# Kernel optimization log

Hardware: AMD Instinct MI355X
Metric: run time of the kernel (lower is better)

The kernel has to match this reference:

```python
import jax, jax.numpy as jnp
import numpy as np
from jax import lax

B, N, C = 256, 256, 192
HEADS = 6
HD = C // HEADS
WIN = 16
AGENT = 49
POOL = 7            # int(agent_num ** 0.5)
SCALE = HD ** -0.5


def _pool_matrix(inn, out):
    # PyTorch AdaptiveAvgPool2d bin edges: start=floor(i*inn/out), end=ceil((i+1)*inn/out)
    P = np.zeros((out, inn), np.float32)
    for i in range(out):
        s = (i * inn) // out
        e = -(((-(i + 1)) * inn) // out)
        P[i, s:e] = 1.0 / (e - s)
    return jnp.asarray(P)

_P = _pool_matrix(WIN, POOL)  # (7, 16) adaptive-avg-pool operator


def _resize_bilinear(x, out_h, out_w):
    # matches F.interpolate(mode='bilinear', align_corners=False)
    H, W = x.shape[-2], x.shape[-1]
    def idx(out, inn):
        s = (jnp.arange(out, dtype=jnp.float32) + 0.5) * (inn / out) - 0.5
        s = jnp.maximum(s, 0.0)
        i0 = jnp.minimum(jnp.floor(s).astype(jnp.int32), inn - 1)
        i1 = jnp.minimum(i0 + 1, inn - 1)
        return i0, i1, s - i0.astype(jnp.float32)
    h0, h1, th = idx(out_h, H)
    w0, w1, tw = idx(out_w, W)
    xh = x[..., h0, :] * (1.0 - th)[:, None] + x[..., h1, :] * th[:, None]
    return xh[..., :, w0] * (1.0 - tw) + xh[..., :, w1] * tw


def setup_inputs() -> dict:
    key = jax.random.key(0)
    ks = jax.random.split(key, 18)
    lin = lambda k: jax.random.normal(k, (C, C), jnp.float32) * 0.02
    zc = jnp.zeros((C,), jnp.float32)
    tn = lambda k, shp: jax.random.normal(k, shp, jnp.float32) * 0.02
    return {
        "x_F1": jax.random.normal(ks[0], (B, N, C), jnp.float32),
        "x_C2": jax.random.normal(ks[1], (B, N, C), jnp.float32),
        "x_C1": jax.random.normal(ks[2], (B, N, C), jnp.float32),
        "Wq": lin(ks[3]), "bq": zc,
        "Wk": lin(ks[4]), "bk": zc,
        "Wv": lin(ks[5]), "bv": zc,
        "Wa1": lin(ks[6]), "ba1": zc,
        "Wa2": lin(ks[7]), "ba2": zc,
        "an_bias": tn(ks[8], (HEADS, AGENT, 7, 7)),
        "na_bias": tn(ks[9], (HEADS, AGENT, 7, 7)),
        "ah_bias": tn(ks[10], (1, HEADS, AGENT, WIN, 1)),
        "aw_bias": tn(ks[11], (1, HEADS, AGENT, 1, WIN)),
        "ha_bias": tn(ks[12], (1, HEADS, WIN, 1, AGENT)),
        "wa_bias": tn(ks[13], (1, HEADS, 1, WIN, AGENT)),
        "dwc_w": tn(ks[14], (C, 1, 3, 3)),
        "dwc_b": zc,
        "Wp": lin(ks[15]), "bp": zc,
    }


def reference(x_F1, x_C2, x_C1, Wq, bq, Wk, bk, Wv, bv, Wa1, ba1, Wa2, ba2,
              an_bias, na_bias, ah_bias, aw_bias, ha_bias, wa_bias,
              dwc_w, dwc_b, Wp, bp):
    b, n, c = x_F1.shape
    h = w = WIN
    q = x_F1 @ Wq.T + bq
    k = (x_F1 + x_C2 - x_C1) @ Wk.T + bk
    v = (x_C2 - x_C1) @ Wv.T + bv
    # agent tokens: linear -> adaptive avg pool 16x16 -> 7x7 -> (b, 49, c)
    a1 = (x_C1 @ Wa1.T + ba1).reshape(b, h, w, c)
    a1 = jnp.einsum('ph,bhwc,qw->bpqc', _P, a1, _P).reshape(b, AGENT, c)
    a2 = (x_C2 @ Wa2.T + ba2).reshape(b, h, w, c)
    a2 = jnp.einsum('ph,bhwc,qw->bpqc', _P, a2, _P).reshape(b, AGENT, c)
    qh = q.reshape(b, n, HEADS, HD).transpose(0, 2, 1, 3)
    kh = k.reshape(b, n, HEADS, HD).transpose(0, 2, 1, 3)
    vh = v.reshape(b, n, HEADS, HD).transpose(0, 2, 1, 3)
    a1h = a1.reshape(b, AGENT, HEADS, HD).transpose(0, 2, 1, 3)
    a2h = a2.reshape(b, AGENT, HEADS, HD).transpose(0, 2, 1, 3)
    # stage 1: agent <- k/v attention, bias = interp(an_bias) + (ah+aw)
    pb = (_resize_bilinear(an_bias, h, w).reshape(1, HEADS, AGENT, n)
          + (ah_bias + aw_bias).reshape(1, HEADS, AGENT, n))
    attn2 = jax.nn.softmax(SCALE * jnp.einsum('bhad,bhnd->bhan', a2h, kh) + pb, axis=-1)
    agent_v = jnp.einsum('bhan,bhnd->bhad', attn2, vh)
    # stage 2: query <- agent attention, bias = interp(na_bias)^T + (ha+wa)
    ab = (jnp.swapaxes(_resize_bilinear(na_bias, h, w).reshape(HEADS, AGENT, n), -1, -2)[None]
          + (ha_bias + wa_bias).reshape(1, HEADS, n, AGENT))
    q_attn = jax.nn.softmax(SCALE * jnp.einsum('bhnd,bhad->bhna', qh, a1h) + ab, axis=-1)
    x = jnp.einsum('bhna,bhad->bhnd', q_attn, agent_v).transpose(0, 2, 1, 3).reshape(b, n, c)
    # depthwise 3x3 conv on q as spatial map
    q_img = q.reshape(b, h, w, c).transpose(0, 3, 1, 2)
    dw = lax.conv_general_dilated(q_img, dwc_w, (1, 1), ((1, 1), (1, 1)),
                                  feature_group_count=c,
                                  dimension_numbers=('NCHW', 'OIHW', 'NCHW'))
    dw = dw + dwc_b.reshape(1, c, 1, 1)
    x = x + dw.transpose(0, 2, 3, 1).reshape(b, n, c)
    return x @ Wp.T + bp
```

## Files before the change

### kernel.cpp

```cpp
#include <hip/hip_runtime.h>

typedef __bf16 bf16;
typedef __bf16 bf16x4 __attribute__((ext_vector_type(4)));
typedef __bf16 bf16x8 __attribute__((ext_vector_type(8)));
typedef float  f32x4  __attribute__((ext_vector_type(4)));

#define DEVI __device__ __forceinline__

static constexpr int   BATCH = 256;
static constexpr int   SEQ   = 256;
static constexpr int   CH    = 192;
static constexpr int   NH    = 6;
static constexpr int   AG    = 49;
static constexpr float QK_SCALE = 0.17677669529663687f;

__device__ constexpr int   PPN[16]  = {1,1,2,1,2,1,2,1,1,2,1,2,1,2,1,1};
__device__ constexpr int   PPB0[16] = {0,0,0,1,1,2,2,3,3,3,4,4,5,5,6,6};
__device__ constexpr int   PPB1[16] = {0,0,1,0,2,0,3,0,0,4,0,5,0,6,0,0};
__device__ constexpr float PPW0[16] = {1.f/3.f,1.f/3.f,1.f/3.f,1.f/3.f,1.f/3.f,1.f/3.f,1.f/3.f,0.25f,0.25f,0.25f,
                                       1.f/3.f,1.f/3.f,1.f/3.f,1.f/3.f,1.f/3.f,1.f/3.f};
__device__ constexpr float PPW1[16] = {0.f,0.f,1.f/3.f,0.f,1.f/3.f,0.f,0.25f,0.f,0.f,1.f/3.f,
                                       0.f,1.f/3.f,0.f,1.f/3.f,0.f,0.f};

#if defined(__has_builtin)
#if __has_builtin(__builtin_amdgcn_global_load_lds)
#define HAVE_GLL 1
#endif
#endif

DEVI void gll16(const void* g, void* l, int lane) {
#ifdef HAVE_GLL
  (void)lane;
  __builtin_amdgcn_global_load_lds(
      (const __attribute__((address_space(1))) void*)g,
      (__attribute__((address_space(3))) void*)l, 16, 0, 0);
#else
  *(uint4*)((char*)l + lane * 16) = *(const uint4*)((const char*)g);
#endif
}

DEVI float bilin7(const float* m, int i, int j) {
  float sh = (i + 0.5f) * 0.4375f - 0.5f; sh = sh < 0.f ? 0.f : sh;
  float sw = (j + 0.5f) * 0.4375f - 0.5f; sw = sw < 0.f ? 0.f : sw;
  int i0 = (int)sh; if (i0 > 6) i0 = 6;
  int j0 = (int)sw; if (j0 > 6) j0 = 6;
  int i1 = i0 + 1;  if (i1 > 6) i1 = 6;
  int j1 = j0 + 1;  if (j1 > 6) j1 = 6;
  float th = sh - (float)i0, tw = sw - (float)j0;
  float v00 = m[i0*7 + j0], v01 = m[i0*7 + j1];
  float v10 = m[i1*7 + j0], v11 = m[i1*7 + j1];
  return (v00*(1.f-tw) + v01*tw)*(1.f-th) + (v10*(1.f-tw) + v11*tw)*th;
}

__global__ void k_prep(const float* Wq, const float* Wk, const float* Wv,
                       const float* Wa1, const float* Wa2, const float* Wp,
                       const float* an_bias, const float* na_bias,
                       const float* ah_bias, const float* aw_bias,
                       const float* ha_bias, const float* wa_bias,
                       bf16* wsW, float* pb, float* ab, bf16* a1, bf16* a2) {
  int gid = blockIdx.x * 256 + threadIdx.x;
  if (gid < 221184) {
    int mi = gid / 36864, r = gid - mi * 36864;
    const float* W = (mi == 0 ? Wq : mi == 1 ? Wk : mi == 2 ? Wv :
                      mi == 3 ? Wa1 : mi == 4 ? Wa2 : Wp);
    wsW[gid] = (bf16)W[r];
  } else if (gid < 296448) {
    int r = gid - 221184;
    int n = r & 255, ha = r >> 8;
    int i = n >> 4, j = n & 15;
    float val = bilin7(an_bias + (size_t)ha * 49, i, j)
              + ah_bias[ha * 16 + i] + aw_bias[ha * 16 + j];
    pb[r] = val;
  } else if (gid < 371712) {
    int r = gid - 296448;
    int a = r % 49, hn = r / 49;
    int n = hn & 255, hh = hn >> 8;
    int i = n >> 4, j = n & 15;
    float val = bilin7(na_bias + (size_t)(hh * 49 + a) * 49, i, j)
              + ha_bias[(hh * 16 + i) * 49 + a] + wa_bias[(hh * 16 + j) * 49 + a];
    ab[r] = val;
  } else if (gid < 396288) {
    int r = gid - 371712;
    if (r < 12288) a1[(size_t)12544 * CH + r] = (bf16)0.f;
    else           a2[(size_t)12544 * CH + (r - 12288)] = (bf16)0.f;
  }
}

__global__ __launch_bounds__(256, 2) void k_qkv(
    const float* xF1, const float* xC2, const float* xC1,
    const bf16* wsW, const float* bq, const float* bk, const float* bv,
    bf16* qO, bf16* kO, bf16* vO) {
  __shared__ char L[73728] __attribute__((aligned(16)));
  const int tid = threadIdx.x, lane = tid & 63, wid = tid >> 6;
  const int l15 = lane & 15, lg = lane >> 4;
  const int m0 = blockIdx.x * 32;

  {
    const char* s0 = (const char*)(xF1 + (size_t)m0 * CH);
    const char* s1 = (const char*)(xC2 + (size_t)m0 * CH);
    const char* s2 = (const char*)(xC1 + (size_t)m0 * CH);
    #pragma unroll
    for (int i = 0; i < 6; ++i) {
      const int off = (wid * 6 + i) * 1024;
      gll16(s0 + off + lane * 16, L + off, lane);
    }
    #pragma unroll
    for (int i = 0; i < 6; ++i) {
      const int off = (wid * 6 + i) * 1024;
      gll16(s1 + off + lane * 16, L + 24576 + off, lane);
    }
    #pragma unroll
    for (int i = 0; i < 6; ++i) {
      const int off = (wid * 6 + i) * 1024;
      gll16(s2 + off + lane * 16, L + 49152 + off, lane);
    }
  }
  __syncthreads();

  {
    float vF[24], v2[24], v1[24];
    #pragma unroll
    for (int g = 0; g < 6; ++g) {
      const int byt = (tid + 256 * g) * 16;
      *(float4*)&vF[4 * g] = *(const float4*)(L + byt);
      *(float4*)&v2[4 * g] = *(const float4*)(L + 24576 + byt);
      *(float4*)&v1[4 * g] = *(const float4*)(L + 49152 + byt);
    }
    __syncthreads();
    #pragma unroll
    for (int g = 0; g < 6; ++g) {
      bf16x4 tq, tk, tv;
      #pragma unroll
      for (int e = 0; e < 4; ++e) {
        const float f = vF[4 * g + e];
        const float d = v2[4 * g + e] - v1[4 * g + e];
        tq[e] = (bf16)f;
        tk[e] = (bf16)(f + d);
        tv[e] = (bf16)d;
      }
      const int f0  = (tid + 256 * g) * 4;
      const int row = f0 / 192, col = f0 - row * 192;
      const int cb2 = col * 2;
      const int byt = row * 384 + ((cb2 & ~15) ^ ((row & 7) << 4)) + (cb2 & 15);
      *(bf16x4*)(L + byt)         = tq;
      *(bf16x4*)(L + 12288 + byt) = tk;
      *(bf16x4*)(L + 24576 + byt) = tv;
    }
  }
  __syncthreads();

  #pragma unroll 1
  for (int job = 0; job < 3; ++job) {
    const bf16*  Wj   = wsW + job * 36864;
    const float* bias = (job == 0 ? bq : job == 1 ? bk : bv);
    bf16*        outp = (job == 0 ? qO : job == 1 ? kO : vO);
    const char*  T    = L + job * 12288;

    f32x4 acc[2][3];
    #pragma unroll
    for (int rt = 0; rt < 2; ++rt)
      #pragma unroll
      for (int ct = 0; ct < 3; ++ct) acc[rt][ct] = f32x4{0.f, 0.f, 0.f, 0.f};

    #pragma unroll
    for (int kk = 0; kk < 6; ++kk) {
      bf16x8 af[2];
      #pragma unroll
      for (int rt = 0; rt < 2; ++rt) {
        const int row = 16 * rt + l15;
        af[rt] = *(const bf16x8*)(T + row * 384 + ((kk * 64 + lg * 16) ^ ((row & 7) << 4)));
      }
      #pragma unroll
      for (int ct = 0; ct < 3; ++ct) {
        const int ncol = 48 * wid + 16 * ct + l15;
        bf16x8 bfr = *(const bf16x8*)&Wj[(size_t)ncol * CH + kk * 32 + 8 * lg];
        acc[0][ct] = __builtin_amdgcn_mfma_f32_16x16x32_bf16(af[0], bfr, acc[0][ct], 0, 0, 0);
        acc[1][ct] = __builtin_amdgcn_mfma_f32_16x16x32_bf16(af[1], bfr, acc[1][ct], 0, 0, 0);
      }
    }
    __syncthreads();
    #pragma unroll
    for (int ct = 0; ct < 3; ++ct) {
      const int col = 48 * wid + 16 * ct + l15;
      const float bb = bias[col];
      #pragma unroll
      for (int rt = 0; rt < 2; ++rt)
        #pragma unroll
        for (int r = 0; r < 4; ++r) {
          const int row = 16 * rt + 4 * lg + r;
          *(bf16*)(L + 36864 + row * 400 + col * 2) = (bf16)(acc[rt][ct][r] + bb);
        }
    }
    __syncthreads();
    #pragma unroll
    for (int v = 0; v < 3; ++v) {
      const int c   = tid + 256 * v;
      const int row = c / 24;
      const int y   = (c - row * 24) * 16;
      bf16x8 vv = *(const bf16x8*)(L + 36864 + row * 400 + y);
      *(bf16x8*)((char*)outp + (size_t)(m0 + row) * 384 + y) = vv;
    }
  }
}

__global__ __launch_bounds__(192) void k_pool(
    const float* xC1, const float* xC2, bf16* pooled1, bf16* pooled2) {
  const int b = blockIdx.x, which = blockIdx.y, c = threadIdx.x;
  const float* src = (which ? xC2 : xC1) + (size_t)b * SEQ * CH + c;
  bf16* dst = (which ? pooled2 : pooled1) + (size_t)b * AG * CH + c;
  float acc[49];
  #pragma unroll
  for (int a = 0; a < 49; ++a) acc[a] = 0.f;
  #pragma unroll
  for (int i = 0; i < 16; ++i) {
    float jq[7] = {0.f, 0.f, 0.f, 0.f, 0.f, 0.f, 0.f};
    #pragma unroll
    for (int j = 0; j < 16; ++j) {
      const float x = src[(i * 16 + j) * CH];
      jq[PPB0[j]] += PPW0[j] * x;
      if (PPN[j] == 2) jq[PPB1[j]] += PPW1[j] * x;
    }
    {
      const int p0 = PPB0[i]; const float w0 = PPW0[i];
      #pragma unroll
      for (int qq = 0; qq < 7; ++qq) acc[p0 * 7 + qq] += w0 * jq[qq];
    }
    if (PPN[i] == 2) {
      const int p1 = PPB1[i]; const float w1 = PPW1[i];
      #pragma unroll
      for (int qq = 0; qq < 7; ++qq) acc[p1 * 7 + qq] += w1 * jq[qq];
    }
  }
  #pragma unroll
  for (int a = 0; a < 49; ++a) dst[(size_t)a * CH + c] = (bf16)acc[a];
}

DEVI void gemm_body(const bf16* Asrc, const bf16* W, const float* bias,
                    bf16* outp, int m0, bf16 (*sA)[72]) {
  const int tid = threadIdx.x, lane = tid & 63, wid = tid >> 6;
  const int l15 = lane & 15, lg = lane >> 4;
  const int wr = wid >> 1, wc = wid & 1;
  const int srow = tid >> 1, shalf = tid & 1;

  f32x4 acc[4][6];
  #pragma unroll
  for (int a = 0; a < 4; ++a)
    #pragma unroll
    for (int b2 = 0; b2 < 6; ++b2) acc[a][b2] = f32x4{0.f, 0.f, 0.f, 0.f};

  for (int ks = 0; ks < 3; ++ks) {
    const int k0 = ks * 64;
    const uint4* src = (const uint4*)(Asrc + (size_t)(m0 + srow) * CH + k0 + shalf * 32);
    #pragma unroll
    for (int i2 = 0; i2 < 4; ++i2)
      *(uint4*)&sA[srow][shalf * 32 + 8 * i2] = src[i2];
    __syncthreads();
    #pragma unroll
    for (int kk = 0; kk < 64; kk += 32) {
      bf16x8 af[4];
      #pragma unroll
      for (int rt = 0; rt < 4; ++rt)
        af[rt] = *(const bf16x8*)&sA[64 * wr + 16 * rt + l15][kk + 8 * lg];
      #pragma unroll
      for (int ct = 0; ct < 6; ++ct) {
        const int ncol = 96 * wc + 16 * ct + l15;
        bf16x8 bfr = *(const bf16x8*)&W[(size_t)ncol * CH + k0 + kk + 8 * lg];
        #pragma unroll
        for (int rt = 0; rt < 4; ++rt)
          acc[rt][ct] = __builtin_amdgcn_mfma_f32_16x16x32_bf16(af[rt], bfr, acc[rt][ct], 0, 0, 0);
      }
    }
    __syncthreads();
  }
  #pragma unroll
  for (int ct = 0; ct < 6; ++ct) {
    const int col = 96 * wc + 16 * ct + l15;
    const float bb = bias[col];
    #pragma unroll
    for (int rt = 0; rt < 4; ++rt) {
      const size_t rbase = (size_t)(m0 + 64 * wr + 16 * rt + 4 * lg);
      #pragma unroll
      for (int r = 0; r < 4; ++r)
        outp[(rbase + r) * CH + col] = (bf16)(acc[rt][ct][r] + bb);
    }
  }
}

__global__ __launch_bounds__(256, 2) void k_gemm2(
    const bf16* pooled1, const bf16* pooled2, const bf16* wsW,
    const float* ba1, const float* ba2, bf16* a1, bf16* a2) {
  __shared__ bf16 sA[128][72] __attribute__((aligned(16)));
  const int m0 = blockIdx.x * 128;
  if (blockIdx.y == 0) gemm_body(pooled1, wsW + 3 * 36864, ba1, a1, m0, sA);
  else                 gemm_body(pooled2, wsW + 4 * 36864, ba2, a2, m0, sA);
}

__global__ __launch_bounds__(256, 3) void k_gemm_out(
    const bf16* xsum, const bf16* Wp, const float* bp, float* out) {
  __shared__ char sA[49152] __attribute__((aligned(16)));
  const int tid = threadIdx.x, lane = tid & 63, wid = tid >> 6;
  const int l15 = lane & 15, lg = lane >> 4;
  const int wr = wid >> 1, wc = wid & 1;
  const int m0 = blockIdx.x * 128;

  {
    const char* gsrc = (const char*)xsum + (size_t)m0 * 384;
    #pragma unroll
    for (int i = 0; i < 12; ++i) {
      const int off = (wid * 12 + i) * 1024;
      gll16(gsrc + off + lane * 16, sA + off, lane);
    }
  }
  __syncthreads();

  f32x4 acc[4][6];
  #pragma unroll
  for (int a = 0; a < 4; ++a)
    #pragma unroll
    for (int b2 = 0; b2 < 6; ++b2) acc[a][b2] = f32x4{0.f, 0.f, 0.f, 0.f};

  #pragma unroll
  for (int kk = 0; kk < 6; ++kk) {
    bf16x8 af[4];
    #pragma unroll
    for (int rt = 0; rt < 4; ++rt) {
      const int row = 64 * wr + 16 * rt + l15;
      af[rt] = *(const bf16x8*)(sA + row * 384 + ((kk * 64 + lg * 16) ^ ((row & 7) << 4)));
    }
    #pragma unroll
    for (int ct = 0; ct < 6; ++ct) {
      const int ncol = 96 * wc + 16 * ct + l15;
      bf16x8 bfr = *(const bf16x8*)&Wp[(size_t)ncol * CH + kk * 32 + 8 * lg];
      #pragma unroll
      for (int rt = 0; rt < 4; ++rt)
        acc[rt][ct] = __builtin_amdgcn_mfma_f32_16x16x32_bf16(af[rt], bfr, acc[rt][ct], 0, 0, 0);
    }
  }
  #pragma unroll
  for (int ct = 0; ct < 6; ++ct) {
    const int col = 96 * wc + 16 * ct + l15;
    const float bb = bp[col];
    #pragma unroll
    for (int rt = 0; rt < 4; ++rt)
      #pragma unroll
      for (int r = 0; r < 4; ++r)
        out[(size_t)(m0 + 64 * wr + 16 * rt + 4 * lg + r) * CH + col] = acc[rt][ct][r] + bb;
  }
}

__global__ __launch_bounds__(256, 2) void k_attn(
    const bf16* q, const bf16* k, const bf16* v,
    const bf16* a1, const bf16* a2, const float* pb, const float* ab,
    const float* dwc_w, const float* dwc_b, bf16* xsum) {
  const int h = blockIdx.x, b = blockIdx.y;
  __shared__ char uSmem[36864] __attribute__((aligned(16)));
  bf16 (*log1)[264] = reinterpret_cast<bf16 (*)[264]>(uSmem);
  bf16 (*log2)[72]  = reinterpret_cast<bf16 (*)[72]>(uSmem);
  __shared__ bf16 sVT[32][264] __attribute__((aligned(16)));
  __shared__ bf16 sAVT[32][72] __attribute__((aligned(16)));
  __shared__ float srow1[64];
  __shared__ float srow2[256];
  __shared__ bf16 xat[256][36] __attribute__((aligned(16)));
  __shared__ float sW[9][32];
  __shared__ float dwb[32];

  const int tid = threadIdx.x, lane = tid & 63, wv = tid >> 6;
  const int l15 = lane & 15, lg = lane >> 4;

  const bf16* qb  = q  + (size_t)b * SEQ * CH + h * 32;
  const bf16* kb  = k  + (size_t)b * SEQ * CH + h * 32;
  const bf16* vb  = v  + (size_t)b * SEQ * CH + h * 32;
  const bf16* a1b = a1 + (size_t)b * AG  * CH + h * 32;
  const bf16* a2b = a2 + (size_t)b * AG  * CH + h * 32;

  for (int idx = tid; idx < 288; idx += 256) {
    const int cl = idx / 9, tap = idx - cl * 9;
    sW[tap][cl] = dwc_w[(32 * h + cl) * 9 + tap];
  }
  if (tid < 32) dwb[tid] = dwc_b[32 * h + tid];

  {
    const int p = tid & 127, dg = tid >> 7;
    const bf16* s0 = vb + (size_t)(2 * p) * CH + dg * 16;
    bf16x8 r0a = ((const bf16x8*)s0)[0];
    bf16x8 r0b = ((const bf16x8*)s0)[1];
    bf16x8 r1a = ((const bf16x8*)(s0 + CH))[0];
    bf16x8 r1b = ((const bf16x8*)(s0 + CH))[1];
    #pragma unroll
    for (int j = 0; j < 8; ++j) {
      union { bf16 e[2]; unsigned u; } u0, u1;
      u0.e[0] = r0a[j]; u0.e[1] = r1a[j];
      u1.e[0] = r0b[j]; u1.e[1] = r1b[j];
      *(unsigned*)&sVT[dg * 16 + j][2 * p]     = u0.u;
      *(unsigned*)&sVT[dg * 16 + 8 + j][2 * p] = u1.u;
    }
  }

  {
    bf16x8 afr[4];
    #pragma unroll
    for (int rt = 0; rt < 4; ++rt)
      afr[rt] = *(const bf16x8*)(a2b + (size_t)(16 * rt + l15) * CH + 8 * lg);
    #pragma unroll
    for (int ct = 0; ct < 4; ++ct) {
      const int n = 64 * wv + 16 * ct + l15;
      bf16x8 bfr = *(const bf16x8*)(kb + (size_t)n * CH + 8 * lg);
      #pragma unroll
      for (int rt = 0; rt < 4; ++rt) {
        f32x4 acc = {0.f, 0.f, 0.f, 0.f};
        acc = __builtin_amdgcn_mfma_f32_16x16x32_bf16(afr[rt], bfr, acc, 0, 0, 0);
        #pragma unroll
        for (int r = 0; r < 4; ++r)
          log1[16 * rt + 4 * lg + r][n] = (bf16)acc[r];
      }
    }
  }
  __syncthreads();

  if (tid < 196) {
    const int a = tid >> 2, qu = tid & 3;
    const float* pbrow = pb + ((size_t)h * AG + a) * SEQ + qu * 64;
    float vbuf[64];
    float m = -1e30f;
    #pragma unroll
    for (int i2 = 0; i2 < 8; ++i2) {
      bf16x8 raw = *(const bf16x8*)&log1[a][qu * 64 + 8 * i2];
      #pragma unroll
      for (int j = 0; j < 8; ++j) {
        float x = QK_SCALE * (float)raw[j] + pbrow[8 * i2 + j];
        vbuf[8 * i2 + j] = x;
        m = fmaxf(m, x);
      }
    }
    m = fmaxf(m, __shfl_xor(m, 1));
    m = fmaxf(m, __shfl_xor(m, 2));
    float s = 0.f;
    #pragma unroll
    for (int i2 = 0; i2 < 8; ++i2) {
      bf16x8 eb;
      #pragma unroll
      for (int j = 0; j < 8; ++j) {
        float e = __expf(vbuf[8 * i2 + j] - m);
        s += e;
        eb[j] = (bf16)e;
      }
      *(bf16x8*)&log1[a][qu * 64 + 8 * i2] = eb;
    }
    s += __shfl_xor(s, 1);
    s += __shfl_xor(s, 2);
    if (qu == 0) srow1[a] = 1.f / s;
  }
  __syncthreads();

  {
    f32x4 acc0 = {0.f, 0.f, 0.f, 0.f}, acc1 = {0.f, 0.f, 0.f, 0.f};
    #pragma unroll
    for (int ksn = 0; ksn < 8; ++ksn) {
      bf16x8 af = *(const bf16x8*)&log1[16 * wv + l15][32 * ksn + 8 * lg];
      bf16x8 b0 = *(const bf16x8*)&sVT[l15][32 * ksn + 8 * lg];
      bf16x8 b1 = *(const bf16x8*)&sVT[16 + l15][32 * ksn + 8 * lg];
      acc0 = __builtin_amdgcn_mfma_f32_16x16x32_bf16(af, b0, acc0, 0, 0, 0);
      acc1 = __builtin_amdgcn_mfma_f32_16x16x32_bf16(af, b1, acc1, 0, 0, 0);
    }
    #pragma unroll
    for (int r = 0; r < 4; ++r) {
      const int a = 16 * wv + 4 * lg + r;
      const float inv = (a < AG) ? srow1[a] : 0.f;
      sAVT[l15][a]      = (bf16)(acc0[r] * inv);
      sAVT[16 + l15][a] = (bf16)(acc1[r] * inv);
    }
  }
  __syncthreads();

  {
    bf16x8 bfr[4];
    #pragma unroll
    for (int ct = 0; ct < 4; ++ct)
      bfr[ct] = *(const bf16x8*)(a1b + (size_t)(16 * ct + l15) * CH + 8 * lg);
    #pragma unroll
    for (int rt = 0; rt < 4; ++rt) {
      bf16x8 af = *(const bf16x8*)(qb + (size_t)(64 * wv + 16 * rt + l15) * CH + 8 * lg);
      #pragma unroll
      for (int ct = 0; ct < 4; ++ct) {
        f32x4 acc = {0.f, 0.f, 0.f, 0.f};
        acc = __builtin_amdgcn_mfma_f32_16x16x32_bf16(af, bfr[ct], acc, 0, 0, 0);
        #pragma unroll
        for (int r = 0; r < 4; ++r)
          log2[64 * wv + 16 * rt + 4 * lg + r][16 * ct + l15] = (bf16)acc[r];
      }
    }
  }
  __syncthreads();

  {
    const float* abrow = ab + ((size_t)h * SEQ + tid) * AG;
    float vb2[49];
    float m = -1e30f;
    #pragma unroll
    for (int i2 = 0; i2 < 6; ++i2) {
      bf16x8 raw = *(const bf16x8*)&log2[tid][8 * i2];
      #pragma unroll
      for (int j = 0; j < 8; ++j) {
        float x = QK_SCALE * (float)raw[j] + abrow[8 * i2 + j];
        vb2[8 * i2 + j] = x;
        m = fmaxf(m, x);
      }
    }
    {
      float x = QK_SCALE * (float)log2[tid][48] + abrow[48];
      vb2[48] = x;
      m = fmaxf(m, x);
    }
    float s = 0.f;
    #pragma unroll
    for (int i2 = 0; i2 < 8; ++i2) {
      bf16x8 eb;
      #pragma unroll
      for (int j = 0; j < 8; ++j) {
        const int idx = 8 * i2 + j;
        float e = 0.f;
        if (idx < AG) { e = __expf(vb2[idx] - m); }
        s += e;
        eb[j] = (bf16)e;
      }
      *(bf16x8*)&log2[tid][8 * i2] = eb;
    }
    srow2[tid] = 1.f / s;
  }
  __syncthreads();

  {
    bf16x8 bfr[2][2];
    #pragma unroll
    for (int ksn = 0; ksn < 2; ++ksn) {
      bfr[ksn][0] = *(const bf16x8*)&sAVT[l15][32 * ksn + 8 * lg];
      bfr[ksn][1] = *(const bf16x8*)&sAVT[16 + l15][32 * ksn + 8 * lg];
    }
    #pragma unroll
    for (int rt = 0; rt < 4; ++rt) {
      f32x4 acc0 = {0.f, 0.f, 0.f, 0.f}, acc1 = {0.f, 0.f, 0.f, 0.f};
      #pragma unroll
      for (int ksn = 0; ksn < 2; ++ksn) {
        bf16x8 af = *(const bf16x8*)&log2[64 * wv + 16 * rt + l15][32 * ksn + 8 * lg];
        acc0 = __builtin_amdgcn_mfma_f32_16x16x32_bf16(af, bfr[ksn][0], acc0, 0, 0, 0);
        acc1 = __builtin_amdgcn_mfma_f32_16x16x32_bf16(af, bfr[ksn][1], acc1, 0, 0, 0);
      }
      #pragma unroll
      for (int r = 0; r < 4; ++r) {
        const int nq = 64 * wv + 16 * rt + 4 * lg + r;
        const float inv = srow2[nq];
        xat[nq][l15]      = (bf16)(acc0[r] * inv);
        xat[nq][16 + l15] = (bf16)(acc1[r] * inv);
      }
    }
  }
  __syncthreads();

  {
    const int n = tid, ii = n >> 4, jj = n & 15;
    float acc[32];
    #pragma unroll
    for (int u = 0; u < 4; ++u) {
      bf16x4 xa0 = *(const bf16x4*)&xat[n][8 * u];
      bf16x4 xa1 = *(const bf16x4*)&xat[n][8 * u + 4];
      #pragma unroll
      for (int e = 0; e < 4; ++e) {
        acc[8 * u + e]     = dwb[8 * u + e]     + (float)xa0[e];
        acc[8 * u + 4 + e] = dwb[8 * u + 4 + e] + (float)xa1[e];
      }
    }
    #pragma unroll
    for (int di = 0; di < 3; ++di) {
      const int i2 = ii + di - 1;
      if ((unsigned)i2 >= 16u) continue;
      #pragma unroll
      for (int dj = 0; dj < 3; ++dj) {
        const int j2 = jj + dj - 1;
        if ((unsigned)j2 >= 16u) continue;
        const int tap = di * 3 + dj;
        const bf16* qr = q + ((size_t)b * SEQ + i2 * 16 + j2) * CH + h * 32;
        #pragma unroll
        for (int u = 0; u < 4; ++u) {
          bf16x8 qv = *(const bf16x8*)(qr + 8 * u);
          const float4* wv4 = (const float4*)&sW[tap][8 * u];
          float4 wa = wv4[0], wb2 = wv4[1];
          acc[8*u+0] += (float)qv[0] * wa.x;  acc[8*u+1] += (float)qv[1] * wa.y;
          acc[8*u+2] += (float)qv[2] * wa.z;  acc[8*u+3] += (float)qv[3] * wa.w;
          acc[8*u+4] += (float)qv[4] * wb2.x; acc[8*u+5] += (float)qv[5] * wb2.y;
          acc[8*u+6] += (float)qv[6] * wb2.z; acc[8*u+7] += (float)qv[7] * wb2.w;
        }
      }
    }
    char* xo = (char*)xsum + (size_t)(b * SEQ + n) * 384;
    const int sw = (n & 7) << 4;
    #pragma unroll
    for (int u = 0; u < 4; ++u) {
      bf16x8 ob;
      #pragma unroll
      for (int e = 0; e < 8; ++e) ob[e] = (bf16)acc[8 * u + e];
      *(bf16x8*)(xo + ((64 * h + 16 * u) ^ sw)) = ob;
    }
  }
}

extern "C" void kernel_launch(void* const* d_in, const int* in_sizes, int n_in,
                              void* d_out, int out_size, void* d_ws, size_t ws_size,
                              hipStream_t stream) {
  (void)in_sizes; (void)n_in; (void)out_size; (void)ws_size;
  const float* xF1 = (const float*)d_in[0];
  const float* xC2 = (const float*)d_in[1];
  const float* xC1 = (const float*)d_in[2];
  const float* Wq  = (const float*)d_in[3];
  const float* bq  = (const float*)d_in[4];
  const float* Wk  = (const float*)d_in[5];
  const float* bk  = (const float*)d_in[6];
  const float* Wv  = (const float*)d_in[7];
  const float* bv  = (const float*)d_in[8];
  const float* Wa1 = (const float*)d_in[9];
  const float* ba1 = (const float*)d_in[10];
  const float* Wa2 = (const float*)d_in[11];
  const float* ba2 = (const float*)d_in[12];
  const float* an_bias = (const float*)d_in[13];
  const float* na_bias = (const float*)d_in[14];
  const float* ah_bias = (const float*)d_in[15];
  const float* aw_bias = (const float*)d_in[16];
  const float* ha_bias = (const float*)d_in[17];
  const float* wa_bias = (const float*)d_in[18];
  const float* dwc_w = (const float*)d_in[19];
  const float* dwc_b = (const float*)d_in[20];
  const float* Wp  = (const float*)d_in[21];
  const float* bp  = (const float*)d_in[22];

  char* ws = (char*)d_ws;
  size_t off = 0;
  auto nxt = [&](size_t bytes) -> char* {
    char* p = ws + off;
    off = (off + bytes + 255) & ~(size_t)255;
    return p;
  };
  const size_t XSZ = (size_t)BATCH * SEQ * CH;
  const size_t ASZ = ((size_t)BATCH * AG + 64) * CH;

  bf16*  wsW     = (bf16*)nxt(6 * 36864 * sizeof(bf16));
  float* pb      = (float*)nxt(6 * 49 * 256 * sizeof(float));
  float* ab      = (float*)nxt(6 * 256 * 49 * sizeof(float));
  bf16*  pooled1 = (bf16*)nxt(ASZ * sizeof(bf16));
  bf16*  pooled2 = (bf16*)nxt(ASZ * sizeof(bf16));
  bf16*  qB      = (bf16*)nxt(XSZ * sizeof(bf16));
  bf16*  kB      = (bf16*)nxt(XSZ * sizeof(bf16));
  bf16*  vB      = (bf16*)nxt(XSZ * sizeof(bf16));
  bf16*  a1B     = (bf16*)nxt(ASZ * sizeof(bf16));
  bf16*  a2B     = (bf16*)nxt(ASZ * sizeof(bf16));
  bf16*  xsum    = (bf16*)nxt(XSZ * sizeof(bf16));

  k_prep<<<1548, 256, 0, stream>>>(Wq, Wk, Wv, Wa1, Wa2, Wp,
                                   an_bias, na_bias, ah_bias, aw_bias,
                                   ha_bias, wa_bias, wsW, pb, ab, a1B, a2B);
  k_qkv<<<2048, 256, 0, stream>>>(xF1, xC2, xC1, wsW, bq, bk, bv, qB, kB, vB);
  k_pool<<<dim3(BATCH, 2), 192, 0, stream>>>(xC1, xC2, pooled1, pooled2);
  k_gemm2<<<dim3(98, 2), 256, 0, stream>>>(pooled1, pooled2, wsW, ba1, ba2, a1B, a2B);
  k_attn<<<dim3(NH, BATCH), 256, 0, stream>>>(qB, kB, vB, a1B, a2B, pb, ab,
                                              dwc_w, dwc_b, xsum);
  k_gemm_out<<<512, 256, 0, stream>>>(xsum, wsW + 5 * 36864, bp, (float*)d_out);
}
```

Baseline: 219.3 us.

## Split QKV projection per job, restructure pooling, store attention biases as bf16

The fused QKV kernel, which staged all three inputs in 72KB of LDS, becomes a per-job projection kernel launched on a 3-deep grid. Each block reads fp32 inputs directly into MFMA fragments and uses a small LDS buffer, which allows higher occupancy. The cost is reading xF1/xC2/xC1 multiple times across jobs. The pooling kernel now processes channel pairs and splits rows across two thread halves, combining them through LDS. The precomputed attention bias tables are stored as bf16 (ab padded to 56) to halve their traffic and allow vector loads, at some precision cost.

```diff
diff --git a/kernel.cpp b/kernel.cpp
--- a/kernel.cpp
+++ b/kernel.cpp
@@ -57,7 +57,7 @@
                        const float* an_bias, const float* na_bias,
                        const float* ah_bias, const float* aw_bias,
                        const float* ha_bias, const float* wa_bias,
-                       bf16* wsW, float* pb, float* ab, bf16* a1, bf16* a2) {
+                       bf16* wsW, bf16* pb, bf16* ab, bf16* a1, bf16* a2) {
   int gid = blockIdx.x * 256 + threadIdx.x;
   if (gid < 221184) {
     int mi = gid / 36864, r = gid - mi * 36864;
@@ -70,169 +70,175 @@
     int i = n >> 4, j = n & 15;
     float val = bilin7(an_bias + (size_t)ha * 49, i, j)
               + ah_bias[ha * 16 + i] + aw_bias[ha * 16 + j];
-    pb[r] = val;
-  } else if (gid < 371712) {
+    pb[r] = (bf16)val;
+  } else if (gid < 382464) {
     int r = gid - 296448;
-    int a = r % 49, hn = r / 49;
+    int a = r % 56, hn = r / 56;
     int n = hn & 255, hh = hn >> 8;
     int i = n >> 4, j = n & 15;
-    float val = bilin7(na_bias + (size_t)(hh * 49 + a) * 49, i, j)
-              + ha_bias[(hh * 16 + i) * 49 + a] + wa_bias[(hh * 16 + j) * 49 + a];
-    ab[r] = val;
-  } else if (gid < 396288) {
-    int r = gid - 371712;
+    float val = 0.f;
+    if (a < AG)
+      val = bilin7(na_bias + (size_t)(hh * 49 + a) * 49, i, j)
+          + ha_bias[(hh * 16 + i) * 49 + a] + wa_bias[(hh * 16 + j) * 49 + a];
+    ab[r] = (bf16)val;
+  } else if (gid < 407040) {
+    int r = gid - 382464;
     if (r < 12288) a1[(size_t)12544 * CH + r] = (bf16)0.f;
     else           a2[(size_t)12544 * CH + (r - 12288)] = (bf16)0.f;
   }
 }
 
-__global__ __launch_bounds__(256, 2) void k_qkv(
+__global__ __launch_bounds__(256, 4) void k_proj(
     const float* xF1, const float* xC2, const float* xC1,
     const bf16* wsW, const float* bq, const float* bk, const float* bv,
     bf16* qO, bf16* kO, bf16* vO) {
-  __shared__ char L[73728] __attribute__((aligned(16)));
+  __shared__ char L[12800] __attribute__((aligned(16)));
   const int tid = threadIdx.x, lane = tid & 63, wid = tid >> 6;
   const int l15 = lane & 15, lg = lane >> 4;
+  const int rh = wid >> 1, chf = wid & 1;
+  const int job = blockIdx.y;
   const int m0 = blockIdx.x * 32;
 
-  {
-    const char* s0 = (const char*)(xF1 + (size_t)m0 * CH);
-    const char* s1 = (const char*)(xC2 + (size_t)m0 * CH);
-    const char* s2 = (const char*)(xC1 + (size_t)m0 * CH);
-    #pragma unroll
-    for (int i = 0; i < 6; ++i) {
-      const int off = (wid * 6 + i) * 1024;
-      gll16(s0 + off + lane * 16, L + off, lane);
-    }
-    #pragma unroll
-    for (int i = 0; i < 6; ++i) {
-      const int off = (wid * 6 + i) * 1024;
-      gll16(s1 + off + lane * 16, L + 24576 + off, lane);
-    }
-    #pragma unroll
-    for (int i = 0; i < 6; ++i) {
-      const int off = (wid * 6 + i) * 1024;
-      gll16(s2 + off + lane * 16, L + 49152 + off, lane);
-    }
-  }
-  __syncthreads();
-
-  {
-    float vF[24], v2[24], v1[24];
-    #pragma unroll
-    for (int g = 0; g < 6; ++g) {
-      const int byt = (tid + 256 * g) * 16;
-      *(float4*)&vF[4 * g] = *(const float4*)(L + byt);
-      *(float4*)&v2[4 * g] = *(const float4*)(L + 24576 + byt);
-      *(float4*)&v1[4 * g] = *(const float4*)(L + 49152 + byt);
-    }
-    __syncthreads();
-    #pragma unroll
-    for (int g = 0; g < 6; ++g) {
-      bf16x4 tq, tk, tv;
-      #pragma unroll
-      for (int e = 0; e < 4; ++e) {
-        const float f = vF[4 * g + e];
-        const float d = v2[4 * g + e] - v1[4 * g + e];
-        tq[e] = (bf16)f;
-        tk[e] = (bf16)(f + d);
-        tv[e] = (bf16)d;
-      }
-      const int f0  = (tid + 256 * g) * 4;
-      const int row = f0 / 192, col = f0 - row * 192;
-      const int cb2 = col * 2;
-      const int byt = row * 384 + ((cb2 & ~15) ^ ((row & 7) << 4)) + (cb2 & 15);
-      *(bf16x4*)(L + byt)         = tq;
-      *(bf16x4*)(L + 12288 + byt) = tk;
-      *(bf16x4*)(L + 24576 + byt) = tv;
-    }
-  }
-  __syncthreads();
-
-  #pragma unroll 1
-  for (int job = 0; job < 3; ++job) {
-    const bf16*  Wj   = wsW + job * 36864;
-    const float* bias = (job == 0 ? bq : job == 1 ? bk : bv);
-    bf16*        outp = (job == 0 ? qO : job == 1 ? kO : vO);
-    const char*  T    = L + job * 12288;
-
-    f32x4 acc[2][3];
-    #pragma unroll
-    for (int rt = 0; rt < 2; ++rt)
-      #pragma unroll
-      for (int ct = 0; ct < 3; ++ct) acc[rt][ct] = f32x4{0.f, 0.f, 0.f, 0.f};
-
-    #pragma unroll
-    for (int kk = 0; kk < 6; ++kk) {
-      bf16x8 af[2];
-      #pragma unroll
-      for (int rt = 0; rt < 2; ++rt) {
-        const int row = 16 * rt + l15;
-        af[rt] = *(const bf16x8*)(T + row * 384 + ((kk * 64 + lg * 16) ^ ((row & 7) << 4)));
-      }
-      #pragma unroll
-      for (int ct = 0; ct < 3; ++ct) {
-        const int ncol = 48 * wid + 16 * ct + l15;
-        bf16x8 bfr = *(const bf16x8*)&Wj[(size_t)ncol * CH + kk * 32 + 8 * lg];
-        acc[0][ct] = __builtin_amdgcn_mfma_f32_16x16x32_bf16(af[0], bfr, acc[0][ct], 0, 0, 0);
-        acc[1][ct] = __builtin_amdgcn_mfma_f32_16x16x32_bf16(af[1], bfr, acc[1][ct], 0, 0, 0);
-      }
-    }
-    __syncthreads();
-    #pragma unroll
-    for (int ct = 0; ct < 3; ++ct) {
-      const int col = 48 * wid + 16 * ct + l15;
-      const float bb = bias[col];
-      #pragma unroll
-      for (int rt = 0; rt < 2; ++rt)
-        #pragma unroll
-        for (int r = 0; r < 4; ++r) {
-          const int row = 16 * rt + 4 * lg + r;
-          *(bf16*)(L + 36864 + row * 400 + col * 2) = (bf16)(acc[rt][ct][r] + bb);
-        }
-    }
-    __syncthreads();
-    #pragma unroll
-    for (int v = 0; v < 3; ++v) {
-      const int c   = tid + 256 * v;
-      const int row = c / 24;
-      const int y   = (c - row * 24) * 16;
-      bf16x8 vv = *(const bf16x8*)(L + 36864 + row * 400 + y);
-      *(bf16x8*)((char*)outp + (size_t)(m0 + row) * 384 + y) = vv;
-    }
-  }
-}
+  const bf16*  Wj   = wsW + job * 36864;
+  const float* bias = (job == 0 ? bq : job == 1 ? bk : bv);
+  bf16*        outp = (job == 0 ? qO : job == 1 ? kO : vO);
+
+  const size_t arow = (size_t)(m0 + 16 * rh + l15) * CH + 8 * lg;
+
+  f32x4 acc[6];
+  #pragma unroll
+  for (int ct = 0; ct < 6; ++ct) acc[ct] = f32x4{0.f, 0.f, 0.f, 0.f};
+
+  #pragma unroll
+  for (int kk = 0; kk < 6; ++kk) {
+    bf16x8 af;
+    if (job == 0) {
+      float f[8];
+      *(float4*)&f[0] = *(const float4*)(xF1 + arow + kk * 32);
+      *(float4*)&f[4] = *(const float4*)(xF1 + arow + kk * 32 + 4);
+      #pragma unroll
+      for (int e = 0; e < 8; ++e) af[e] = (bf16)f[e];
+    } else if (job == 1) {
+      float f[8], c2[8], c1[8];
+      *(float4*)&f[0]  = *(const float4*)(xF1 + arow + kk * 32);
+      *(float4*)&f[4]  = *(const float4*)(xF1 + arow + kk * 32 + 4);
+      *(float4*)&c2[0] = *(const float4*)(xC2 + arow + kk * 32);
+      *(float4*)&c2[4] = *(const float4*)(xC2 + arow + kk * 32 + 4);
+      *(float4*)&c1[0] = *(const float4*)(xC1 + arow + kk * 32);
+      *(float4*)&c1[4] = *(const float4*)(xC1 + arow + kk * 32 + 4);
+      #pragma unroll
+      for (int e = 0; e < 8; ++e) af[e] = (bf16)(f[e] + c2[e] - c1[e]);
+    } else {
+      float c2[8], c1[8];
+      *(float4*)&c2[0] = *(const float4*)(xC2 + arow + kk * 32);
+      *(float4*)&c2[4] = *(const float4*)(xC2 + arow + kk * 32 + 4);
+      *(float4*)&c1[0] = *(const float4*)(xC1 + arow + kk * 32);
+      *(float4*)&c1[4] = *(const float4*)(xC1 + arow + kk * 32 + 4);
+      #pragma unroll
+      for (int e = 0; e < 8; ++e) af[e] = (bf16)(c2[e] - c1[e]);
+    }
+    #pragma unroll
+    for (int ct = 0; ct < 6; ++ct) {
+      const int ncol = 96 * chf + 16 * ct + l15;
+      bf16x8 bfr = *(const bf16x8*)&Wj[(size_t)ncol * CH + kk * 32 + 8 * lg];
+      acc[ct] = __builtin_amdgcn_mfma_f32_16x16x32_bf16(af, bfr, acc[ct], 0, 0, 0);
+    }
+  }
+
+  #pragma unroll
+  for (int ct = 0; ct < 6; ++ct) {
+    const int col = 96 * chf + 16 * ct + l15;
+    const float bb = bias[col];
+    #pragma unroll
+    for (int r = 0; r < 4; ++r)
+      *(bf16*)(L + (16 * rh + 4 * lg + r) * 400 + col * 2) = (bf16)(acc[ct][r] + bb);
+  }
+  __syncthreads();
+  #pragma unroll
+  for (int v = 0; v < 3; ++v) {
+    const int c   = tid + 256 * v;
+    const int row = c / 24;
+    const int y   = (c - row * 24) * 16;
+    *(bf16x8*)((char*)outp + (size_t)(m0 + row) * 384 + y) =
+        *(const bf16x8*)(L + row * 400 + y);
+  }
+}
+
+#define POOLROW(I, P0, W0, P1, W1) do {                                        \
+    float jqx[7] = {0,0,0,0,0,0,0}, jqy[7] = {0,0,0,0,0,0,0};                  \
+    _Pragma("unroll")                                                          \
+    for (int j = 0; j < 16; ++j) {                                             \
+      float2 x = *(const float2*)(src + (size_t)((I) * 16 + j) * CH);          \
+      jqx[PPB0[j]] += PPW0[j] * x.x;  jqy[PPB0[j]] += PPW0[j] * x.y;           \
+      if (PPN[j] == 2) { jqx[PPB1[j]] += PPW1[j] * x.x;                        \
+                         jqy[PPB1[j]] += PPW1[j] * x.y; }                      \
+    }                                                                          \
+    _Pragma("unroll")                                                          \
+    for (int q = 0; q < 7; ++q) { ax[P0][q] += (W0) * jqx[q];                  \
+                                  ay[P0][q] += (W0) * jqy[q]; }                \
+    if ((P1) >= 0) {                                                           \
+      _Pragma("unroll")                                                        \
+      for (int q = 0; q < 7; ++q) { ax[(P1) & 3][q] += (W1) * jqx[q];          \
+                                    ay[(P1) & 3][q] += (W1) * jqy[q]; }        \
+    }                                                                          \
+  } while (0)
 
 __global__ __launch_bounds__(192) void k_pool(
     const float* xC1, const float* xC2, bf16* pooled1, bf16* pooled2) {
-  const int b = blockIdx.x, which = blockIdx.y, c = threadIdx.x;
-  const float* src = (which ? xC2 : xC1) + (size_t)b * SEQ * CH + c;
-  bf16* dst = (which ? pooled2 : pooled1) + (size_t)b * AG * CH + c;
-  float acc[49];
-  #pragma unroll
-  for (int a = 0; a < 49; ++a) acc[a] = 0.f;
-  #pragma unroll
-  for (int i = 0; i < 16; ++i) {
-    float jq[7] = {0.f, 0.f, 0.f, 0.f, 0.f, 0.f, 0.f};
-    #pragma unroll
-    for (int j = 0; j < 16; ++j) {
-      const float x = src[(i * 16 + j) * CH];
-      jq[PPB0[j]] += PPW0[j] * x;
-      if (PPN[j] == 2) jq[PPB1[j]] += PPW1[j] * x;
-    }
-    {
-      const int p0 = PPB0[i]; const float w0 = PPW0[i];
-      #pragma unroll
-      for (int qq = 0; qq < 7; ++qq) acc[p0 * 7 + qq] += w0 * jq[qq];
-    }
-    if (PPN[i] == 2) {
-      const int p1 = PPB1[i]; const float w1 = PPW1[i];
-      #pragma unroll
-      for (int qq = 0; qq < 7; ++qq) acc[p1 * 7 + qq] += w1 * jq[qq];
-    }
-  }
-  #pragma unroll
-  for (int a = 0; a < 49; ++a) dst[(size_t)a * CH + c] = (bf16)acc[a];
+  __shared__ float lred[7][192];
+  const int b = blockIdx.x, which = blockIdx.y, t = threadIdx.x;
+  const int cp = t % 96, ih = t / 96;
+  const float* src = (which ? xC2 : xC1) + (size_t)b * SEQ * CH + 2 * cp;
+  bf16* dst = (which ? pooled2 : pooled1) + (size_t)b * AG * CH + 2 * cp;
+
+  float ax[4][7], ay[4][7];
+  #pragma unroll
+  for (int p = 0; p < 4; ++p)
+    #pragma unroll
+    for (int q = 0; q < 7; ++q) { ax[p][q] = 0.f; ay[p][q] = 0.f; }
+
+  const float TH = 1.f / 3.f, QU = 0.25f;
+  if (ih == 0) {
+    POOLROW(0, 0, TH, -1, 0.f);  POOLROW(1, 0, TH, -1, 0.f);
+    POOLROW(2, 0, TH,  1, TH);   POOLROW(3, 1, TH, -1, 0.f);
+    POOLROW(4, 1, TH,  2, TH);   POOLROW(5, 2, TH, -1, 0.f);
+    POOLROW(6, 2, TH,  3, QU);   POOLROW(7, 3, QU, -1, 0.f);
+  } else {
+    POOLROW(8,  0, QU, -1, 0.f); POOLROW(9,  0, QU,  1, TH);
+    POOLROW(10, 1, TH, -1, 0.f); POOLROW(11, 1, TH,  2, TH);
+    POOLROW(12, 2, TH, -1, 0.f); POOLROW(13, 2, TH,  3, TH);
+    POOLROW(14, 3, TH, -1, 0.f); POOLROW(15, 3, TH, -1, 0.f);
+  }
+  if (ih == 1) {
+    #pragma unroll
+    for (int q = 0; q < 7; ++q) {
+      lred[q][2 * cp] = ax[0][q]; lred[q][2 * cp + 1] = ay[0][q];
+    }
+  }
+  __syncthreads();
+  if (ih == 0) {
+    #pragma unroll
+    for (int q = 0; q < 7; ++q) {
+      ax[3][q] += lred[q][2 * cp]; ay[3][q] += lred[q][2 * cp + 1];
+    }
+    #pragma unroll
+    for (int p = 0; p < 4; ++p)
+      #pragma unroll
+      for (int q = 0; q < 7; ++q) {
+        union { bf16 e[2]; unsigned u; } u;
+        u.e[0] = (bf16)ax[p][q]; u.e[1] = (bf16)ay[p][q];
+        *(unsigned*)&dst[(size_t)(p * 7 + q) * CH] = u.u;
+      }
+  } else {
+    #pragma unroll
+    for (int lp = 1; lp < 4; ++lp)
+      #pragma unroll
+      for (int q = 0; q < 7; ++q) {
+        union { bf16 e[2]; unsigned u; } u;
+        u.e[0] = (bf16)ax[lp][q]; u.e[1] = (bf16)ay[lp][q];
+        *(unsigned*)&dst[(size_t)((3 + lp) * 7 + q) * CH] = u.u;
+      }
+  }
 }
 
 DEVI void gemm_body(const bf16* Asrc, const bf16* W, const float* bias,
@@ -350,7 +356,7 @@
 
 __global__ __launch_bounds__(256, 2) void k_attn(
     const bf16* q, const bf16* k, const bf16* v,
-    const bf16* a1, const bf16* a2, const float* pb, const float* ab,
+    const bf16* a1, const bf16* a2, const bf16* pb, const bf16* ab,
     const float* dwc_w, const float* dwc_b, bf16* xsum) {
   const int h = blockIdx.x, b = blockIdx.y;
   __shared__ char uSmem[36864] __attribute__((aligned(16)));
@@ -419,15 +425,16 @@
 
   if (tid < 196) {
     const int a = tid >> 2, qu = tid & 3;
-    const float* pbrow = pb + ((size_t)h * AG + a) * SEQ + qu * 64;
+    const bf16* pbrow = pb + ((size_t)h * AG + a) * SEQ + qu * 64;
     float vbuf[64];
     float m = -1e30f;
     #pragma unroll
     for (int i2 = 0; i2 < 8; ++i2) {
       bf16x8 raw = *(const bf16x8*)&log1[a][qu * 64 + 8 * i2];
+      bf16x8 pbb = *(const bf16x8*)&pbrow[8 * i2];
       #pragma unroll
       for (int j = 0; j < 8; ++j) {
-        float x = QK_SCALE * (float)raw[j] + pbrow[8 * i2 + j];
+        float x = QK_SCALE * (float)raw[j] + (float)pbb[j];
         vbuf[8 * i2 + j] = x;
         m = fmaxf(m, x);
       }
@@ -493,21 +500,22 @@
   __syncthreads();
 
   {
-    const float* abrow = ab + ((size_t)h * SEQ + tid) * AG;
+    const bf16* abrow = ab + ((size_t)h * SEQ + tid) * 56;
     float vb2[49];
     float m = -1e30f;
     #pragma unroll
     for (int i2 = 0; i2 < 6; ++i2) {
       bf16x8 raw = *(const bf16x8*)&log2[tid][8 * i2];
+      bf16x8 abb = *(const bf16x8*)&abrow[8 * i2];
       #pragma unroll
       for (int j = 0; j < 8; ++j) {
-        float x = QK_SCALE * (float)raw[j] + abrow[8 * i2 + j];
+        float x = QK_SCALE * (float)raw[j] + (float)abb[j];
         vb2[8 * i2 + j] = x;
         m = fmaxf(m, x);
       }
     }
     {
-      float x = QK_SCALE * (float)log2[tid][48] + abrow[48];
+      float x = QK_SCALE * (float)log2[tid][48] + (float)abrow[48];
       vb2[48] = x;
       m = fmaxf(m, x);
     }
@@ -642,8 +650,8 @@
   const size_t ASZ = ((size_t)BATCH * AG + 64) * CH;
 
   bf16*  wsW     = (bf16*)nxt(6 * 36864 * sizeof(bf16));
-  float* pb      = (float*)nxt(6 * 49 * 256 * sizeof(float));
-  float* ab      = (float*)nxt(6 * 256 * 49 * sizeof(float));
+  bf16*  pb      = (bf16*)nxt(6 * 49 * 256 * sizeof(bf16));
+  bf16*  ab      = (bf16*)nxt(6 * 256 * 56 * sizeof(bf16));
   bf16*  pooled1 = (bf16*)nxt(ASZ * sizeof(bf16));
   bf16*  pooled2 = (bf16*)nxt(ASZ * sizeof(bf16));
   bf16*  qB      = (bf16*)nxt(XSZ * sizeof(bf16));
@@ -653,10 +661,11 @@
   bf16*  a2B     = (bf16*)nxt(ASZ * sizeof(bf16));
   bf16*  xsum    = (bf16*)nxt(XSZ * sizeof(bf16));
 
-  k_prep<<<1548, 256, 0, stream>>>(Wq, Wk, Wv, Wa1, Wa2, Wp,
+  k_prep<<<1590, 256, 0, stream>>>(Wq, Wk, Wv, Wa1, Wa2, Wp,
                                    an_bias, na_bias, ah_bias, aw_bias,
                                    ha_bias, wa_bias, wsW, pb, ab, a1B, a2B);
-  k_qkv<<<2048, 256, 0, stream>>>(xF1, xC2, xC1, wsW, bq, bk, bv, qB, kB, vB);
+  k_proj<<<dim3(2048, 3), 256, 0, stream>>>(xF1, xC2, xC1, wsW, bq, bk, bv,
+                                            qB, kB, vB);
   k_pool<<<dim3(BATCH, 2), 192, 0, stream>>>(xC1, xC2, pooled1, pooled2);
   k_gemm2<<<dim3(98, 2), 256, 0, stream>>>(pooled1, pooled2, wsW, ba1, ba2, a1B, a2B);
   k_attn<<<dim3(NH, BATCH), 256, 0, stream>>>(qB, kB, vB, a1B, a2B, pb, ab,
```

Measured after the change: 308.4 us. +40.7%, slower.
